# Performance work log

Measured on AMD Instinct MI355X. Metric: run time of the kernel, lower is better.

Reference implementation:

```python
import math
import jax, jax.numpy as jnp
import numpy as np

K = 7  # kernel_size
PAD = 3  # padding (kernel_size//2)


def _base_kernels():
    # 4 oriented anisotropic Gaussian kernels, [4, K, K]
    sigma1, sigma2 = 2.5, 1.0
    ax = jnp.linspace(-(K // 2), K // 2, K)
    xx, yy = jnp.meshgrid(ax, ax, indexing='ij')
    ks = []
    for theta in (0.0, math.pi / 4, math.pi / 2, 3 * math.pi / 4):
        c, s = math.cos(theta), math.sin(theta)
        x_rot = xx * c + yy * s
        y_rot = -xx * s + yy * c
        k = jnp.exp(-(x_rot ** 2 / (2 * sigma1 ** 2) + y_rot ** 2 / (2 * sigma2 ** 2)))
        ks.append(k / k.sum())
    return jnp.stack(ks, axis=0)


def setup_inputs() -> dict:
    key = jax.random.key(0)
    ks = jax.random.split(key, 8)
    B, C, H, W, mid = 2, 256, 256, 256, 16
    x = jax.random.normal(ks[0], (B, C, H, W), dtype=jnp.float32)
    angle_map = jax.random.uniform(ks[1], (B, H, W), dtype=jnp.float32) * math.pi
    reduce_w = jax.random.normal(ks[2], (mid, C), dtype=jnp.float32) * (1.0 / math.sqrt(C))
    expand_w = jax.random.normal(ks[3], (C, mid), dtype=jnp.float32) * (1.0 / math.sqrt(mid))
    w1 = jax.random.normal(ks[4], (8, 2), dtype=jnp.float32) * (1.0 / math.sqrt(2))
    b1 = jnp.zeros((8,), dtype=jnp.float32)
    w2 = jax.random.normal(ks[5], (4, 8), dtype=jnp.float32) * (1.0 / math.sqrt(8))
    b2 = jnp.zeros((4,), dtype=jnp.float32)
    return {"x": x, "angle_map": angle_map, "reduce_w": reduce_w,
            "expand_w": expand_w, "w1": w1, "b1": b1, "w2": w2, "b2": b2}


def reference(x, angle_map, reduce_w, expand_w, w1, b1, w2, b2):
    B, C, H, W = x.shape
    mid = reduce_w.shape[0]
    base = _base_kernels()  # [4,K,K], constant buffer

    # 1x1 reduce conv
    x_low = jnp.einsum('bchw,mc->bmhw', x, reduce_w)  # [B,mid,H,W]

    # per-pixel mixing weights from angle: MLP(2->8->4) + softmax
    angle_feat = jnp.stack([jnp.sin(2 * angle_map), jnp.cos(2 * angle_map)], axis=-1)  # [B,H,W,2]
    h = jax.nn.relu(jnp.einsum('bhwi,oi->bhwo', angle_feat, w1) + b1)
    weights = jax.nn.softmax(jnp.einsum('bhwi,oi->bhwo', h, w2) + b2, axis=-1)  # [B,H,W,4]

    # reflect pad, then cross-correlate each channel with the 4 base kernels.
    # Equivalent to the original unfold+einsum: out = sum_k w_k * (x_low * base_k)
    x_pad = jnp.pad(x_low, ((0, 0), (0, 0), (PAD, PAD), (PAD, PAD)), mode='reflect')
    Hp, Wp = x_pad.shape[-2:]
    y = jax.lax.conv_general_dilated(
        x_pad.reshape(B * mid, 1, Hp, Wp), base[:, None],  # [4,1,K,K]
        window_strides=(1, 1), padding='VALID')  # [B*mid,4,H,W]
    y = y.reshape(B, mid, 4, H, W)

    out_low = jnp.einsum('bmkhw,bhwk->bmhw', y, weights)  # [B,mid,H,W]
    out = jnp.einsum('bmhw,cm->bchw', out_low, expand_w)  # 1x1 expand conv
    return out
```

## Files before the change

kernel.cpp:

```cpp
#include <hip/hip_runtime.h>

#define H_   256
#define W_   256
#define HW_  65536
#define C_   256
#define MID  16
#define B_   2

__global__ __launch_bounds__(256) void k0_prep(float* __restrict__ base_out) {
    __shared__ float s_k[4][49];
    __shared__ float s_inv[4];
    int t = threadIdx.x;
    if (t < 196) {
        int k = t / 49, p = t % 49;
        int i = p / 7, j = p % 7;
        float xx = (float)(i - 3), yy = (float)(j - 3);
        const float cs[4] = {1.0f, 0.70710678118654752f, 0.0f, -0.70710678118654752f};
        const float sn[4] = {0.0f, 0.70710678118654752f, 1.0f, 0.70710678118654752f};
        float c = cs[k], s = sn[k];
        float xr = xx * c + yy * s;
        float yr = -xx * s + yy * c;
        float v = expf(-(xr * xr * 0.08f + yr * yr * 0.5f));
        s_k[k][p] = v;
    }
    __syncthreads();
    if (t < 4) {
        float s = 0.f;
        for (int p = 0; p < 49; ++p) s += s_k[t][p];
        s_inv[t] = 1.0f / s;
    }
    __syncthreads();
    if (t < 196) base_out[t] = s_k[t / 49][t % 49] * s_inv[t / 49];
}

__global__ __launch_bounds__(256, 2) void kA_reduce(const float* __restrict__ x,
                                                    const float* __restrict__ rw,
                                                    float* __restrict__ xlow) {
    int bh = blockIdx.x;
    int b = bh >> 8, h = bh & 255;
    int w = threadIdx.x;
    const float* xp = x + (size_t)b * C_ * HW_ + h * W_ + w;
    float acc[MID];
#pragma unroll
    for (int m = 0; m < MID; ++m) acc[m] = 0.f;
    for (int cb = 0; cb < C_; cb += 16) {
        float xv[16];
#pragma unroll
        for (int i = 0; i < 16; ++i)
            xv[i] = xp[(size_t)(cb + i) * HW_];
#pragma unroll
        for (int i = 0; i < 16; ++i) {
#pragma unroll
            for (int m = 0; m < MID; ++m)
                acc[m] = fmaf(rw[m * C_ + cb + i], xv[i], acc[m]);
        }
    }
    float* op = xlow + (size_t)b * MID * HW_ + h * W_ + w;
#pragma unroll
    for (int m = 0; m < MID; ++m) op[(size_t)m * HW_] = acc[m];
}

__global__ __launch_bounds__(256, 4) void kB_conv(const float* __restrict__ xlow,
                                                  const float* __restrict__ base,
                                                  const float* __restrict__ angle,
                                                  const float* __restrict__ w1,
                                                  const float* __restrict__ b1,
                                                  const float* __restrict__ w2,
                                                  const float* __restrict__ b2,
                                                  float* __restrict__ olow) {
    int bid = blockIdx.x;
    int mh = bid & 1;
    int h = (bid >> 1) & 255;
    int b = bid >> 9;
    int w = threadIdx.x;

    float a2 = 2.0f * angle[(size_t)b * HW_ + h * W_ + w];
    float f0 = __sinf(a2), f1 = __cosf(a2);
    float hb[8];
#pragma unroll
    for (int j = 0; j < 8; ++j)
        hb[j] = fmaxf(fmaf(w1[j * 2], f0, fmaf(w1[j * 2 + 1], f1, b1[j])), 0.f);
    float lg[4];
#pragma unroll
    for (int k = 0; k < 4; ++k) {
        float s = b2[k];
#pragma unroll
        for (int j = 0; j < 8; ++j) s = fmaf(w2[k * 8 + j], hb[j], s);
        lg[k] = s;
    }
    float mx = fmaxf(fmaxf(lg[0], lg[1]), fmaxf(lg[2], lg[3]));
    float wk[4];
    float ssum = 0.f;
#pragma unroll
    for (int k = 0; k < 4; ++k) { wk[k] = __expf(lg[k] - mx); ssum += wk[k]; }
    float inv = 1.0f / ssum;
#pragma unroll
    for (int k = 0; k < 4; ++k) wk[k] *= inv;

    float e[49];
#pragma unroll
    for (int tp = 0; tp < 49; ++tp)
        e[tp] = fmaf(wk[0], base[tp],
                fmaf(wk[1], base[49 + tp],
                fmaf(wk[2], base[98 + tp], wk[3] * base[147 + tp])));

    int cc[7];
#pragma unroll
    for (int dx = 0; dx < 7; ++dx) {
        int c0 = w + dx - 3;
        cc[dx] = c0 < 0 ? -c0 : (c0 > 255 ? 510 - c0 : c0);
    }
    int rr[7];
#pragma unroll
    for (int dy = 0; dy < 7; ++dy) {
        int hy = h + dy - 3;
        rr[dy] = (hy < 0 ? -hy : (hy > 255 ? 510 - hy : hy)) * W_;
    }

    const float* xb = xlow + (size_t)b * MID * HW_ + (size_t)mh * 8 * HW_;
    float acc[8];
#pragma unroll
    for (int m = 0; m < 8; ++m) {
        const float* pm = xb + (size_t)m * HW_;
        float s = 0.f;
#pragma unroll
        for (int dy = 0; dy < 7; ++dy) {
            const float* r = pm + rr[dy];
#pragma unroll
            for (int dx = 0; dx < 7; ++dx)
                s = fmaf(e[dy * 7 + dx], r[cc[dx]], s);
        }
        acc[m] = s;
    }

    float4* op = (float4*)(olow + ((size_t)b * HW_ + h * W_ + w) * MID + mh * 8);
    op[0] = make_float4(acc[0], acc[1], acc[2], acc[3]);
    op[1] = make_float4(acc[4], acc[5], acc[6], acc[7]);
}

__global__ __launch_bounds__(256) void kC_expand(const float* __restrict__ olow,
                                                 const float* __restrict__ ew,
                                                 float* __restrict__ out) {
    int bid = blockIdx.x;
    int cq = bid & 3;
    int h = (bid >> 2) & 255;
    int b = bid >> 10;
    int w = threadIdx.x;
    const float4* ip = (const float4*)(olow + ((size_t)b * HW_ + h * W_ + w) * MID);
    float4 m0 = ip[0], m1 = ip[1], m2 = ip[2], m3 = ip[3];
    float* ob = out + ((size_t)b * C_ + cq * 64) * HW_ + h * W_ + w;
    const float* wb = ew + (size_t)cq * 64 * MID;
#pragma unroll 8
    for (int ci = 0; ci < 64; ++ci) {
        const float* wc = wb + ci * MID;
        float s;
        s = wc[0] * m0.x;
        s = fmaf(wc[1], m0.y, s);
        s = fmaf(wc[2], m0.z, s);
        s = fmaf(wc[3], m0.w, s);
        s = fmaf(wc[4], m1.x, s);
        s = fmaf(wc[5], m1.y, s);
        s = fmaf(wc[6], m1.z, s);
        s = fmaf(wc[7], m1.w, s);
        s = fmaf(wc[8], m2.x, s);
        s = fmaf(wc[9], m2.y, s);
        s = fmaf(wc[10], m2.z, s);
        s = fmaf(wc[11], m2.w, s);
        s = fmaf(wc[12], m3.x, s);
        s = fmaf(wc[13], m3.y, s);
        s = fmaf(wc[14], m3.z, s);
        s = fmaf(wc[15], m3.w, s);
        __builtin_nontemporal_store(s, ob + (size_t)ci * HW_);
    }
}

extern "C" void kernel_launch(void* const* d_in, const int* in_sizes, int n_in,
                              void* d_out, int out_size, void* d_ws, size_t ws_size,
                              hipStream_t stream) {
    const float* x     = (const float*)d_in[0];
    const float* angle = (const float*)d_in[1];
    const float* rw    = (const float*)d_in[2];
    const float* ew    = (const float*)d_in[3];
    const float* w1    = (const float*)d_in[4];
    const float* b1    = (const float*)d_in[5];
    const float* w2    = (const float*)d_in[6];
    const float* b2    = (const float*)d_in[7];
    float* out = (float*)d_out;

    float* wsf  = (float*)d_ws;
    float* base = wsf;
    float* xlow = wsf + 256;
    float* olow = xlow + (size_t)B_ * MID * HW_;

    hipLaunchKernelGGL(k0_prep,   dim3(1),    dim3(256), 0, stream, base);
    hipLaunchKernelGGL(kA_reduce, dim3(512),  dim3(256), 0, stream, x, rw, xlow);
    hipLaunchKernelGGL(kB_conv,   dim3(1024), dim3(256), 0, stream,
                       xlow, base, angle, w1, b1, w2, b2, olow);
    hipLaunchKernelGGL(kC_expand, dim3(2048), dim3(256), 0, stream, olow, ew, out);
}
```

Before: 336.4 us.

## Split reduce conv over channel quarters with float4 pixels and a separate sum pass

The 1x1 reduce kernel now splits the 256 input channels into four quarters. Each thread handles four pixels with float4 loads, writes partial results to a new workspace buffer, and a new kS_sum kernel adds the four partials into xlow. The aim is more memory-level parallelism and wider loads on the dominant read of x. The cost is an extra kernel launch plus roughly 4x the xlow size in extra traffic. The intermediate olow layout also changes from pixel-major (16 floats per pixel) to channel-planar, so the conv and expand kernels now use coalesced per-channel accesses instead of float4 interleaved ones.

```diff
diff --git a/kernel.cpp b/kernel.cpp
--- a/kernel.cpp
+++ b/kernel.cpp
@@ -35,29 +35,55 @@
 
 __global__ __launch_bounds__(256, 2) void kA_reduce(const float* __restrict__ x,
                                                     const float* __restrict__ rw,
-                                                    float* __restrict__ xlow) {
-    int bh = blockIdx.x;
-    int b = bh >> 8, h = bh & 255;
-    int w = threadIdx.x;
-    const float* xp = x + (size_t)b * C_ * HW_ + h * W_ + w;
-    float acc[MID];
-#pragma unroll
-    for (int m = 0; m < MID; ++m) acc[m] = 0.f;
-    for (int cb = 0; cb < C_; cb += 16) {
-        float xv[16];
-#pragma unroll
-        for (int i = 0; i < 16; ++i)
-            xv[i] = xp[(size_t)(cb + i) * HW_];
-#pragma unroll
-        for (int i = 0; i < 16; ++i) {
-#pragma unroll
-            for (int m = 0; m < MID; ++m)
-                acc[m] = fmaf(rw[m * C_ + cb + i], xv[i], acc[m]);
+                                                    float* __restrict__ part) {
+    int bid = blockIdx.x;
+    int cq = bid & 3;
+    int b = (bid >> 2) & 1;
+    int rg = bid >> 3;
+    int t = threadIdx.x;
+    int px0 = rg * 1024 + t * 4;
+    const float4* xp = (const float4*)(x + (size_t)b * C_ * HW_ + (size_t)cq * 64 * HW_ + px0);
+    const float* wp = rw + cq * 64;
+    float4 acc[MID];
+#pragma unroll
+    for (int m = 0; m < MID; ++m) acc[m] = make_float4(0.f, 0.f, 0.f, 0.f);
+    for (int cb = 0; cb < 64; cb += 8) {
+        float4 xv[8];
+#pragma unroll
+        for (int i = 0; i < 8; ++i)
+            xv[i] = xp[(size_t)(cb + i) * (HW_ / 4)];
+#pragma unroll
+        for (int i = 0; i < 8; ++i) {
+#pragma unroll
+            for (int m = 0; m < MID; ++m) {
+                float wv = wp[m * C_ + cb + i];
+                acc[m].x = fmaf(wv, xv[i].x, acc[m].x);
+                acc[m].y = fmaf(wv, xv[i].y, acc[m].y);
+                acc[m].z = fmaf(wv, xv[i].z, acc[m].z);
+                acc[m].w = fmaf(wv, xv[i].w, acc[m].w);
+            }
         }
     }
-    float* op = xlow + (size_t)b * MID * HW_ + h * W_ + w;
-#pragma unroll
-    for (int m = 0; m < MID; ++m) op[(size_t)m * HW_] = acc[m];
+    float4* op = (float4*)(part + ((size_t)(cq * 2 + b) * MID) * HW_ + px0);
+#pragma unroll
+    for (int m = 0; m < MID; ++m) op[m * (HW_ / 4)] = acc[m];
+}
+
+__global__ __launch_bounds__(256) void kS_sum(const float* __restrict__ part,
+                                              float* __restrict__ xlow) {
+    size_t i = (size_t)blockIdx.x * 256 + threadIdx.x;
+    const size_t stride = (size_t)B_ * MID * HW_ / 4;
+    const float4* p = (const float4*)part;
+    float4 a = p[i];
+    float4 b = p[i + stride];
+    float4 c = p[i + 2 * stride];
+    float4 d = p[i + 3 * stride];
+    float4 r;
+    r.x = (a.x + b.x) + (c.x + d.x);
+    r.y = (a.y + b.y) + (c.y + d.y);
+    r.z = (a.z + b.z) + (c.z + d.z);
+    r.w = (a.w + b.w) + (c.w + d.w);
+    ((float4*)xlow)[i] = r;
 }
 
 __global__ __launch_bounds__(256, 4) void kB_conv(const float* __restrict__ xlow,
@@ -133,9 +159,9 @@
         acc[m] = s;
     }
 
-    float4* op = (float4*)(olow + ((size_t)b * HW_ + h * W_ + w) * MID + mh * 8);
-    op[0] = make_float4(acc[0], acc[1], acc[2], acc[3]);
-    op[1] = make_float4(acc[4], acc[5], acc[6], acc[7]);
+    float* op = olow + ((size_t)b * MID + mh * 8) * HW_ + h * W_ + w;
+#pragma unroll
+    for (int m = 0; m < 8; ++m) op[(size_t)m * HW_] = acc[m];
 }
 
 __global__ __launch_bounds__(256) void kC_expand(const float* __restrict__ olow,
@@ -146,30 +172,18 @@
     int h = (bid >> 2) & 255;
     int b = bid >> 10;
     int w = threadIdx.x;
-    const float4* ip = (const float4*)(olow + ((size_t)b * HW_ + h * W_ + w) * MID);
-    float4 m0 = ip[0], m1 = ip[1], m2 = ip[2], m3 = ip[3];
+    const float* ip = olow + (size_t)b * MID * HW_ + h * W_ + w;
+    float mv[MID];
+#pragma unroll
+    for (int m = 0; m < MID; ++m) mv[m] = ip[(size_t)m * HW_];
     float* ob = out + ((size_t)b * C_ + cq * 64) * HW_ + h * W_ + w;
     const float* wb = ew + (size_t)cq * 64 * MID;
 #pragma unroll 8
     for (int ci = 0; ci < 64; ++ci) {
         const float* wc = wb + ci * MID;
-        float s;
-        s = wc[0] * m0.x;
-        s = fmaf(wc[1], m0.y, s);
-        s = fmaf(wc[2], m0.z, s);
-        s = fmaf(wc[3], m0.w, s);
-        s = fmaf(wc[4], m1.x, s);
-        s = fmaf(wc[5], m1.y, s);
-        s = fmaf(wc[6], m1.z, s);
-        s = fmaf(wc[7], m1.w, s);
-        s = fmaf(wc[8], m2.x, s);
-        s = fmaf(wc[9], m2.y, s);
-        s = fmaf(wc[10], m2.z, s);
-        s = fmaf(wc[11], m2.w, s);
-        s = fmaf(wc[12], m3.x, s);
-        s = fmaf(wc[13], m3.y, s);
-        s = fmaf(wc[14], m3.z, s);
-        s = fmaf(wc[15], m3.w, s);
+        float s = wc[0] * mv[0];
+#pragma unroll
+        for (int m = 1; m < MID; ++m) s = fmaf(wc[m], mv[m], s);
         __builtin_nontemporal_store(s, ob + (size_t)ci * HW_);
     }
 }
@@ -191,9 +205,11 @@
     float* base = wsf;
     float* xlow = wsf + 256;
     float* olow = xlow + (size_t)B_ * MID * HW_;
+    float* part = olow + (size_t)B_ * MID * HW_;
 
     hipLaunchKernelGGL(k0_prep,   dim3(1),    dim3(256), 0, stream, base);
-    hipLaunchKernelGGL(kA_reduce, dim3(512),  dim3(256), 0, stream, x, rw, xlow);
+    hipLaunchKernelGGL(kA_reduce, dim3(512),  dim3(256), 0, stream, x, rw, part);
+    hipLaunchKernelGGL(kS_sum,    dim3(2048), dim3(256), 0, stream, part, xlow);
     hipLaunchKernelGGL(kB_conv,   dim3(1024), dim3(256), 0, stream,
                        xlow, base, angle, w1, b1, w2, b2, olow);
     hipLaunchKernelGGL(kC_expand, dim3(2048), dim3(256), 0, stream, olow, ew, out);
```

Measured after the change: 340.1 us. No clear change (+1.1%).
